# Kernel tuning notes

Hardware: AMD Instinct MI355X
Metric: run time of the kernel (lower is better)

Reference implementation:

```python
import jax, jax.numpy as jnp
import numpy as np
from jax import lax

B, T, C = 1, 2048, 2048
HS = 64
H = C // HS          # 32 heads
FFN = 7168
NS = 4               # packed sequences in the batch-1 stream
EPS_LN = 1e-5
EPS_GN = 1e-5 * 8 ** 2   # GroupNorm eps = 1e-5 * head_size_divisor**2


def setup_inputs() -> dict:
    key = jax.random.key(0)
    ks = iter(jax.random.split(key, 48))
    def rn(shape, s=1.0):
        return jax.random.normal(next(ks), shape, jnp.float32) * s
    sc = C ** -0.5
    return dict(
        x=rn((B, T, C)),
        start_pos=jnp.array([0, 512, 1024, 1536], dtype=jnp.int32),
        att_state=rn((NS, C)),
        wkv_state=rn((NS, H, HS, HS), 0.1),
        ffn_state=rn((NS, C)),
        ln1_g=jnp.ones((C,), jnp.float32), ln1_b=jnp.zeros((C,), jnp.float32),
        ln2_g=jnp.ones((C,), jnp.float32), ln2_b=jnp.zeros((C,), jnp.float32),
        tm_maa_x=rn((C,), 0.1), tm_maa_w=rn((C,), 0.1), tm_maa_k=rn((C,), 0.1),
        tm_maa_v=rn((C,), 0.1), tm_maa_r=rn((C,), 0.1), tm_maa_g=rn((C,), 0.1),
        tm_w1=rn((C, 160), 0.02), tm_w2=rn((5, 32, C), 0.02),
        td=rn((C,), 0.3) - 0.5, td_w1=rn((C, 64), 0.02), td_w2=rn((64, C), 0.02),
        u=rn((H, HS), 0.1),
        Wr=rn((C, C), sc), Wk=rn((C, C), sc), Wv=rn((C, C), sc),
        Wg=rn((C, C), sc), Wo=rn((C, C), sc),
        lnx_g=jnp.ones((C,), jnp.float32), lnx_b=jnp.zeros((C,), jnp.float32),
        cm_maa_k=rn((C,), 0.1), cm_maa_r=rn((C,), 0.1),
        Wck=rn((C, FFN), sc), Wcv=rn((FFN, C), FFN ** -0.5), Wcr=rn((C, C), sc),
    )


def _ln(x, g, b, eps):
    m = x.mean(-1, keepdims=True)
    v = ((x - m) ** 2).mean(-1, keepdims=True)
    return (x - m) * lax.rsqrt(v + eps) * g + b


def _shift(x, start_pos, state):
    # ZeroPad2d((0,0,1,-1)) token shift, then restore per-sequence carry state
    sh = jnp.concatenate([jnp.zeros_like(x[:, :1]), x[:, :-1]], axis=1)
    return sh.at[0, start_pos, :].set(state)


def reference(x, start_pos, att_state, wkv_state, ffn_state,
              ln1_g, ln1_b, ln2_g, ln2_b,
              tm_maa_x, tm_maa_w, tm_maa_k, tm_maa_v, tm_maa_r, tm_maa_g,
              tm_w1, tm_w2, td, td_w1, td_w2, u,
              Wr, Wk, Wv, Wg, Wo, lnx_g, lnx_b,
              cm_maa_k, cm_maa_r, Wck, Wcv, Wcr):
    is_start = jnp.zeros((T,), bool).at[start_pos].set(True)
    seq_id = jnp.clip(jnp.cumsum(is_start.astype(jnp.int32)) - 1, 0, NS - 1)

    # ---------------- Tmix (RWKV6 time mix) ----------------
    xa = _ln(x, ln1_g, ln1_b, EPS_LN)
    sh = _shift(xa, start_pos, att_state)
    xx = sh - xa
    xxx = jnp.tanh((xa + xx * tm_maa_x) @ tm_w1)                    # [B,T,160]
    mix = jnp.einsum('btse,sec->sbtc', xxx.reshape(B, T, 5, 32), tm_w2)
    mw, mk, mv, mr, mg = mix
    xw = xa + xx * (tm_maa_w + mw)
    xk = xa + xx * (tm_maa_k + mk)
    xv = xa + xx * (tm_maa_v + mv)
    xr = xa + xx * (tm_maa_r + mr)
    xg = xa + xx * (tm_maa_g + mg)
    r = (xr @ Wr).reshape(T, H, HS)
    k = (xk @ Wk).reshape(T, H, HS)
    v = (xv @ Wv).reshape(T, H, HS)
    g = jax.nn.silu(xg @ Wg)                                        # [B,T,C]
    w = td + jnp.tanh(xw @ td_w1) @ td_w2                           # [B,T,C]
    dec = jnp.exp(-jnp.exp(w)).reshape(T, H, HS)

    # continuous WKV recurrence: per-sequence state restore at starts
    def step(S, inp):
        rt, kt, vt, dt, st, sid = inp
        S = jnp.where(st, wkv_state[sid], S)                        # [H,HS,HS]
        y = jnp.einsum('hi,hij->hj', rt, S) \
            + (rt * u * kt).sum(-1, keepdims=True) * vt             # bonus term
        S = dt[:, :, None] * S + kt[:, :, None] * vt[:, None, :]
        return S, y

    _, y = lax.scan(step, jnp.zeros((H, HS, HS), jnp.float32),
                    (r, k, v, dec, is_start, seq_id))
    y = y.reshape(B, T, H, HS)
    # GroupNorm (n_head groups) fused per token/head
    mu = y.mean(-1, keepdims=True)
    var = ((y - mu) ** 2).mean(-1, keepdims=True)
    y = ((y - mu) * lax.rsqrt(var + EPS_GN)).reshape(B, T, C) * lnx_g + lnx_b
    x = x + (y * g) @ Wo

    # ---------------- CMix (channel mix) ----------------
    xf = _ln(x, ln2_g, ln2_b, EPS_LN)
    sh = _shift(xf, start_pos, ffn_state)
    xx = sh - xf
    xk = xf + xx * cm_maa_k
    xr = xf + xx * cm_maa_r
    kv = jnp.square(jax.nn.relu(xk @ Wck)) @ Wcv
    x = x + jax.nn.sigmoid(xr @ Wcr) * kv
    return x
```

## Files before the change

### kernel.cpp

```cpp
#include <hip/hip_runtime.h>
#include <stdint.h>


#define TT 2048
#define CC 2048
#define NH 32
#define HSZ 64
#define FFND 7168
#define CHUNK 32
#define NCHUNK 64

typedef __attribute__((ext_vector_type(8))) short short8;
typedef __attribute__((ext_vector_type(4))) float f32x4;

__device__ __forceinline__ float bf2f(short s){
  return __uint_as_float(((uint32_t)(uint16_t)s) << 16);
}
__device__ __forceinline__ short f2bf(float f){
  uint32_t u = __float_as_uint(f);
  u = u + 0x7fffu + ((u >> 16) & 1u);
  return (short)(u >> 16);
}

__global__ __launch_bounds__(256) void ln_kernel(
    const float* __restrict__ xin, const float* __restrict__ gam,
    const float* __restrict__ bet, float* __restrict__ out, float eps)
{
  int t = blockIdx.x, tid = threadIdx.x;
  const float* row = xin + (size_t)t*CC;
  float4 v0 = *(const float4*)(row + tid*8);
  float4 v1 = *(const float4*)(row + tid*8 + 4);
  float s  = v0.x+v0.y+v0.z+v0.w + v1.x+v1.y+v1.z+v1.w;
  float ss = v0.x*v0.x+v0.y*v0.y+v0.z*v0.z+v0.w*v0.w
           + v1.x*v1.x+v1.y*v1.y+v1.z*v1.z+v1.w*v1.w;
  #pragma unroll
  for(int off=1; off<64; off<<=1){ s += __shfl_xor(s,off); ss += __shfl_xor(ss,off); }
  __shared__ float sm[8];
  int w = tid>>6;
  if((tid&63)==0){ sm[w]=s; sm[4+w]=ss; }
  __syncthreads();
  s = sm[0]+sm[1]+sm[2]+sm[3]; ss = sm[4]+sm[5]+sm[6]+sm[7];
  float mean = s * (1.f/CC);
  float var  = ss * (1.f/CC) - mean*mean;
  float rstd = rsqrtf(var + eps);
  float* orow = out + (size_t)t*CC;
  int c = tid*8;
  float vv[8] = {v0.x,v0.y,v0.z,v0.w,v1.x,v1.y,v1.z,v1.w};
  #pragma unroll
  for(int j=0;j<8;j++) orow[c+j] = (vv[j]-mean)*rstd*gam[c+j] + bet[c+j];
}

__global__ __launch_bounds__(256) void ln2_fused_kernel(
    const float* __restrict__ p0, const float* __restrict__ p1,
    const float* __restrict__ xres, const float* __restrict__ gam,
    const float* __restrict__ bet, float* __restrict__ xsum,
    float* __restrict__ lnout, float eps)
{
  int t = blockIdx.x, tid = threadIdx.x;
  size_t base = (size_t)t*CC + tid*8;
  float vv[8];
  float s = 0.f, ss = 0.f;
  #pragma unroll
  for(int j=0;j<8;j++){
    float v = p0[base+j] + p1[base+j] + xres[base+j];
    vv[j] = v; s += v; ss += v*v;
    xsum[base+j] = v;
  }
  #pragma unroll
  for(int off=1; off<64; off<<=1){ s += __shfl_xor(s,off); ss += __shfl_xor(ss,off); }
  __shared__ float sm[8];
  int w = tid>>6;
  if((tid&63)==0){ sm[w]=s; sm[4+w]=ss; }
  __syncthreads();
  s = sm[0]+sm[1]+sm[2]+sm[3]; ss = sm[4]+sm[5]+sm[6]+sm[7];
  float mean = s * (1.f/CC);
  float var  = ss * (1.f/CC) - mean*mean;
  float rstd = rsqrtf(var + eps);
  int c = tid*8;
  #pragma unroll
  for(int j=0;j<8;j++) lnout[base+j] = (vv[j]-mean)*rstd*gam[c+j] + bet[c+j];
}

__global__ __launch_bounds__(256) void shift1_kernel(
    const float* __restrict__ xa, const float* __restrict__ st,
    const int* __restrict__ sp, float* __restrict__ xxb)
{
  int t = blockIdx.x, tid = threadIdx.x;
  int sp0=sp[0], sp1=sp[1], sp2=sp[2], sp3=sp[3];
  bool is_start = (sp0==t)|(sp1==t)|(sp2==t)|(sp3==t);
  int sid = (sp0<=t)+(sp1<=t)+(sp2<=t)+(sp3<=t) - 1;
  sid = sid<0?0:(sid>3?3:sid);
  int c = tid*8;
  const float* src = is_start ? (st + (size_t)sid*CC + c)
                   : (t>0 ? xa + (size_t)(t-1)*CC + c : nullptr);
  const float* cur = xa + (size_t)t*CC + c;
  float* o = xxb + (size_t)t*CC + c;
  #pragma unroll
  for(int jj=0;jj<8;jj++){
    float sh = src ? src[jj] : 0.f;
    o[jj] = sh - cur[jj];
  }
}

__global__ __launch_bounds__(256) void shift2_kernel(
    const float* __restrict__ xf, const float* __restrict__ st,
    const int* __restrict__ sp, const float* __restrict__ cmk,
    const float* __restrict__ cmr, short* __restrict__ xk2, short* __restrict__ xr2)
{
  int t = blockIdx.x, tid = threadIdx.x;
  int sp0=sp[0], sp1=sp[1], sp2=sp[2], sp3=sp[3];
  bool is_start = (sp0==t)|(sp1==t)|(sp2==t)|(sp3==t);
  int sid = (sp0<=t)+(sp1<=t)+(sp2<=t)+(sp3<=t) - 1;
  sid = sid<0?0:(sid>3?3:sid);
  int c = tid*8;
  const float* src = is_start ? (st + (size_t)sid*CC + c)
                   : (t>0 ? xf + (size_t)(t-1)*CC + c : nullptr);
  const float* cur = xf + (size_t)t*CC + c;
  size_t ix = (size_t)t*CC + c;
  #pragma unroll
  for(int jj=0;jj<8;jj++){
    float xfv = cur[jj];
    float sh = src ? src[jj] : 0.f;
    float d = sh - xfv;
    xk2[ix+jj] = f2bf(xfv + d*cmk[c+jj]);
    xr2[ix+jj] = f2bf(xfv + d*cmr[c+jj]);
  }
}

__global__ __launch_bounds__(256) void zprep_kernel(const float* __restrict__ xa,
   const float* __restrict__ xx, const float* __restrict__ maa, short* __restrict__ z)
{
  size_t i = ((size_t)blockIdx.x*256 + threadIdx.x)*8;
  int c = (int)(i & (CC-1));
  #pragma unroll
  for(int j=0;j<8;j++) z[i+j] = f2bf(xa[i+j] + xx[i+j]*maa[c+j]);
}

__global__ __launch_bounds__(256) void mix5_kernel(
    const float* __restrict__ xxxb, const float* __restrict__ w2,
    const float* __restrict__ xa, const float* __restrict__ xxv,
    const float* __restrict__ mw, const float* __restrict__ mk,
    const float* __restrict__ mv, const float* __restrict__ mr,
    const float* __restrict__ mg,
    short* __restrict__ ow, short* __restrict__ ok, short* __restrict__ ov,
    short* __restrict__ orr, short* __restrict__ og)
{
  int g = blockIdx.x*256 + threadIdx.x;
  int c = g & (CC-1);
  int t0 = (g >> 11) * 8;
  float acc[5][8];
  #pragma unroll
  for(int s=0;s<5;s++)
    #pragma unroll
    for(int tt=0;tt<8;tt++) acc[s][tt]=0.f;
  #pragma unroll
  for(int s=0;s<5;s++){
    for(int e=0;e<32;e++){
      float wv = w2[(size_t)(s*32+e)*CC + c];
      #pragma unroll
      for(int tt=0;tt<8;tt++)
        acc[s][tt] += xxxb[(size_t)(t0+tt)*160 + s*32 + e] * wv;
    }
  }
  float vmw=mw[c], vmk=mk[c], vmv=mv[c], vmr=mr[c], vmg=mg[c];
  #pragma unroll
  for(int tt=0;tt<8;tt++){
    size_t ix = (size_t)(t0+tt)*CC + c;
    float av = xa[ix], xv = xxv[ix];
    ow[ix]  = f2bf(av + xv*(vmw + acc[0][tt]));
    ok[ix]  = f2bf(av + xv*(vmk + acc[1][tt]));
    ov[ix]  = f2bf(av + xv*(vmv + acc[2][tt]));
    orr[ix] = f2bf(av + xv*(vmr + acc[3][tt]));
    og[ix]  = f2bf(av + xv*(vmg + acc[4][tt]));
  }
}

__global__ __launch_bounds__(256) void dec_kernel(
    const float* __restrict__ h1b, const float* __restrict__ tw2,
    const float* __restrict__ td, float* __restrict__ out)
{
  int g = blockIdx.x*256 + threadIdx.x;
  int c = g & (CC-1);
  int t0 = (g >> 11)*8;
  float acc[8] = {0,0,0,0,0,0,0,0};
  for(int e=0;e<64;e++){
    float wv = tw2[(size_t)e*CC + c];
    #pragma unroll
    for(int tt=0;tt<8;tt++) acc[tt] += h1b[(size_t)(t0+tt)*64 + e]*wv;
  }
  float tdc = td[c];
  #pragma unroll
  for(int tt=0;tt<8;tt++)
    out[(size_t)(t0+tt)*CC + c] = expf(-expf(tdc + acc[tt]));
}

template<int N, int NK>
__global__ __launch_bounds__(256) void tanh_reduce_kernel(
    const float* __restrict__ part, float* __restrict__ out)
{
  int idx = blockIdx.x*256 + threadIdx.x;
  int col = idx & (N-1);
  int row = idx >> (N==256 ? 8 : 7);
  float s = 0.f;
  #pragma unroll
  for(int z=0;z<8;z++) s += part[(size_t)z*TT*N + idx];
  if(col < NK) out[(size_t)row*NK + col] = tanhf(s);
}

__global__ __launch_bounds__(256) void transpose_f2bf_kernel(
    const float* __restrict__ W, short* __restrict__ Wt, int K, int N)
{
  __shared__ float tile[64][65];
  int n0 = blockIdx.x*64, k0 = blockIdx.y*64;
  int tid = threadIdx.x;
  #pragma unroll
  for(int q=0;q<16;q++){
    int ix = q*256 + tid;
    int r = ix >> 6, cc2 = ix & 63;
    tile[r][cc2] = (n0 + cc2 < N) ? W[(size_t)(k0+r)*N + n0 + cc2] : 0.f;
  }
  __syncthreads();
  #pragma unroll
  for(int q=0;q<16;q++){
    int ix = q*256 + tid;
    int r = ix >> 6, cc2 = ix & 63;
    Wt[(size_t)(n0+r)*K + k0 + cc2] = f2bf(tile[cc2][r]);
  }
}

struct WPtr4 { const float* w[4]; };
__global__ __launch_bounds__(256) void transpose4_f2bf_kernel(
    WPtr4 ws4, short* __restrict__ Wt)
{
  __shared__ float tile[64][65];
  int z = blockIdx.z;
  const float* W = ws4.w[z];
  short* dst = Wt + (size_t)z*CC*CC;
  int n0 = blockIdx.x*64, k0 = blockIdx.y*64;
  int tid = threadIdx.x;
  #pragma unroll
  for(int q=0;q<16;q++){
    int ix = q*256 + tid;
    int r = ix >> 6, cc2 = ix & 63;
    tile[r][cc2] = W[(size_t)(k0+r)*CC + n0 + cc2];
  }
  __syncthreads();
  #pragma unroll
  for(int q=0;q<16;q++){
    int ix = q*256 + tid;
    int r = ix >> 6, cc2 = ix & 63;
    dst[(size_t)(n0+r)*CC + k0 + cc2] = f2bf(tile[cc2][r]);
  }
}

__device__ __forceinline__ void load_lds16(const void* g, void* l){
  __builtin_amdgcn_global_load_lds(
      (const __attribute__((address_space(1))) uint32_t*)g,
      (__attribute__((address_space(3))) uint32_t*)l, 16, 0, 0);
}

template<int EPI>
__global__ __launch_bounds__(256) void gemm_bt_kernel(
    const short* __restrict__ A, const short* __restrict__ Bt,
    void* __restrict__ Cout, int M, int N, int Kstride, int Klen,
    long zA, long zB, long zC)
{
  __shared__ __align__(16) short As[128*64];
  __shared__ __align__(16) short Bs[128*64];
  int z = blockIdx.z;
  const short* A0 = A + (size_t)z*zA;
  const short* B0 = Bt + (size_t)z*zB;
  int tid = threadIdx.x;
  int w = tid >> 6, lane = tid & 63;
  int l16 = lane & 15, lhi = lane >> 4;
  int wr = w >> 1, wc = w & 1;
  int gx = gridDim.x;
  int nwg = gx*gridDim.y;
  int lin = blockIdx.y*gx + blockIdx.x;
  int wg = (lin & 7)*(nwg >> 3) + (lin >> 3);
  int bn = wg % gx, bm = wg / gx;
  const short* Ab = A0 + (size_t)bm*128*Kstride;
  const short* Bb = B0 + (size_t)bn*128*Kstride;
  int srow = w*8 + (lane>>3);
  int scol = lane & 7;
  f32x4 acc[4][4] = {};
  for(int kt=0; kt<Klen; kt+=64){
    __syncthreads();
    #pragma unroll
    for(int q=0;q<4;q++){
      int row = q*32 + srow;
      int c8 = scol ^ (row & 7);
      int ldsoff = (q*256 + w*64)*8;
      load_lds16(Ab + (size_t)row*Kstride + kt + c8*8, As + ldsoff);
      load_lds16(Bb + (size_t)row*Kstride + kt + c8*8, Bs + ldsoff);
    }
    __syncthreads();
    #pragma unroll
    for(int kk=0;kk<2;kk++){
      short8 af[4], bf[4];
      #pragma unroll
      for(int m=0;m<4;m++){
        int row = wr*64 + m*16 + l16;
        int slot = (kk*4 + lhi) ^ (row & 7);
        af[m] = *(const short8*)(As + row*64 + slot*8);
      }
      #pragma unroll
      for(int n=0;n<4;n++){
        int row = wc*64 + n*16 + l16;
        int slot = (kk*4 + lhi) ^ (row & 7);
        bf[n] = *(const short8*)(Bs + row*64 + slot*8);
      }
      #pragma unroll
      for(int m=0;m<4;m++){
        #pragma unroll
        for(int n=0;n<4;n++)
          acc[m][n] = __builtin_amdgcn_mfma_f32_16x16x32_bf16(af[m], bf[n], acc[m][n], 0, 0, 0);
      }
    }
  }
  int m0 = bm*128 + wr*64;
  int n0 = bn*128 + wc*64;
  #pragma unroll
  for(int m=0;m<4;m++){
    #pragma unroll
    for(int n=0;n<4;n++){
      #pragma unroll
      for(int jj=0;jj<4;jj++){
        int row = m0 + m*16 + lhi*4 + jj;
        int col = n0 + n*16 + l16;
        size_t ix = (size_t)row*N + col;
        float val = acc[m][n][jj];
        if constexpr (EPI==0){ ((short*)Cout)[(size_t)z*zC + ix] = f2bf(val); }
        else if constexpr (EPI==3){ float rv = fmaxf(val, 0.f); ((short*)Cout)[ix] = f2bf(rv*rv); }
        else if constexpr (EPI==5){ ((float*)Cout)[(size_t)z*zC + ix] = val; }
        else {
          short* o = (short*)Cout + (size_t)z*zC;
          o[ix] = (z==3) ? f2bf(val/(1.f+expf(-val))) : f2bf(val);
        }
      }
    }
  }
}

template<int EPI>
__global__ __launch_bounds__(512, 1) void gemm256_kernel(
    const short* __restrict__ A, const short* __restrict__ Bt,
    void* __restrict__ Cout, int M, int N, int Kstride, int Klen,
    long zA, long zB, long zC)
{
  __shared__ __align__(16) short As[2][256*64];
  __shared__ __align__(16) short Bs[2][256*64];
  int z = blockIdx.z;
  const short* A0 = A + (size_t)z*zA;
  const short* B0 = Bt + (size_t)z*zB;
  int tid = threadIdx.x;
  int w = tid >> 6, lane = tid & 63;
  int l16 = lane & 15, lhi = lane >> 4;
  int wr = w >> 2, wc = w & 3;
  int gx = gridDim.x;
  int nwg = gx*gridDim.y;
  int lin = blockIdx.y*gx + blockIdx.x;
  int wg = (lin & 7)*(nwg >> 3) + (lin >> 3);
  int bn = wg % gx, bm = wg / gx;
  const short* Ab = A0 + (size_t)bm*256*Kstride;
  const short* Bb = B0 + (size_t)bn*256*Kstride;
  int srow_w = w*8 + (lane>>3);
  int scol = lane & 7;
  f32x4 acc[8][4] = {};

  auto STAGE = [&](int kt, int b){
    #pragma unroll
    for(int q=0;q<4;q++){
      int row = q*64 + srow_w;
      int c8 = scol ^ (row & 7);
      int ldsoff = (q*64 + w*8)*64;
      load_lds16(Ab + (size_t)row*Kstride + kt + c8*8, &As[b][ldsoff]);
      load_lds16(Bb + (size_t)row*Kstride + kt + c8*8, &Bs[b][ldsoff]);
    }
  };

  int NT = Klen >> 6;
  int cur = 0;
  STAGE(0, 0);
  for(int t=0; t<NT; ++t){
    __builtin_amdgcn_sched_barrier(0);
    if(t+1 < NT){
      STAGE((t+1)<<6, cur^1);
      asm volatile("s_waitcnt vmcnt(8)" ::: "memory");
    } else {
      asm volatile("s_waitcnt vmcnt(0)" ::: "memory");
    }
    __builtin_amdgcn_s_barrier();
    __builtin_amdgcn_sched_barrier(0);
    const short* Ac = &As[cur][0];
    const short* Bc = &Bs[cur][0];
    short8 bfr[4][2];
    #pragma unroll
    for(int n=0;n<4;n++){
      #pragma unroll
      for(int kk=0;kk<2;kk++){
        int row = wc*64 + n*16 + l16;
        int slot = (kk*4 + lhi) ^ (row & 7);
        bfr[n][kk] = *(const short8*)(Bc + row*64 + slot*8);
      }
    }
    #pragma unroll
    for(int p=0;p<4;p++){
      short8 afr[2][2];
      #pragma unroll
      for(int mm=0;mm<2;mm++){
        #pragma unroll
        for(int kk=0;kk<2;kk++){
          int row = wr*128 + (p*2+mm)*16 + l16;
          int slot = (kk*4 + lhi) ^ (row & 7);
          afr[mm][kk] = *(const short8*)(Ac + row*64 + slot*8);
        }
      }
      __builtin_amdgcn_s_setprio(1);
      #pragma unroll
      for(int mm=0;mm<2;mm++){
        #pragma unroll
        for(int n=0;n<4;n++){
          #pragma unroll
          for(int kk=0;kk<2;kk++)
            acc[p*2+mm][n] = __builtin_amdgcn_mfma_f32_16x16x32_bf16(
                afr[mm][kk], bfr[n][kk], acc[p*2+mm][n], 0, 0, 0);
        }
      }
      __builtin_amdgcn_s_setprio(0);
      __builtin_amdgcn_s_barrier();
    }
    cur ^= 1;
  }
  int m0 = bm*256 + wr*128;
  int n0 = bn*256 + wc*64;
  #pragma unroll
  for(int m=0;m<8;m++){
    #pragma unroll
    for(int n=0;n<4;n++){
      #pragma unroll
      for(int jj=0;jj<4;jj++){
        int row = m0 + m*16 + lhi*4 + jj;
        int col = n0 + n*16 + l16;
        size_t ix = (size_t)row*N + col;
        float val = acc[m][n][jj];
        if constexpr (EPI==3){ float rv = fmaxf(val, 0.f); ((short*)Cout)[ix] = f2bf(rv*rv); }
        else if constexpr (EPI==5){ ((float*)Cout)[(size_t)z*zC + ix] = val; }
        else {
          short* o = (short*)Cout + (size_t)z*zC;
          o[ix] = (z==3) ? f2bf(val/(1.f+expf(-val))) : f2bf(val);
        }
      }
    }
  }
}

__global__ __launch_bounds__(256) void wkv_chunk_kernel(
    const short* __restrict__ rb, const short* __restrict__ kb,
    const short* __restrict__ vb, const float* __restrict__ db,
    const float* __restrict__ wkv_state, const float* __restrict__ u,
    const int* __restrict__ sp,
    float* __restrict__ yb, short* __restrict__ rtb,
    float* __restrict__ Bc, float* __restrict__ Pc)
{
  int blk = blockIdx.x;
  int ch = blk >> 5;
  int h  = blk & 31;
  int tid = threadIdx.x;
  int a = tid & 3, j = tid >> 2;
  int w = tid >> 6, lane = tid & 63;
  __shared__ float sr[2][64], sk[2][64], suk[2][64], sv[2][64], sd[2][64];
  __shared__ float sp_[64];
  float u_reg = (w==1) ? u[h*64 + lane] : 0.f;
  if(tid < 64) sp_[tid] = 1.f;
  float S[16];
  #pragma unroll
  for(int ii=0;ii<16;ii++) S[ii]=0.f;
  int sp0=sp[0], sp1=sp[1], sp2=sp[2], sp3=sp[3];
  int tbase = ch*CHUNK;
  {
    size_t gb = (size_t)tbase*CC + h*64;
    if(w==0)      sr[0][lane] = bf2f(rb[gb+lane]);
    else if(w==1){ float kv_=bf2f(kb[gb+lane]); sk[0][lane]=kv_; suk[0][lane]=u_reg*kv_; }
    else if(w==2) sv[0][lane] = bf2f(vb[gb+lane]);
    else          sd[0][lane] = db[gb+lane];
  }
  __syncthreads();
  for(int tl=0; tl<CHUNK; ++tl){
    int t = tbase + tl;
    int buf = tl & 1;
    if(tl+1 < CHUNK){
      size_t nb = (size_t)(t+1)*CC + h*64;
      int b2_ = buf^1;
      if(w==0)      sr[b2_][lane] = bf2f(rb[nb+lane]);
      else if(w==1){ float kv_=bf2f(kb[nb+lane]); sk[b2_][lane]=kv_; suk[b2_][lane]=u_reg*kv_; }
      else if(w==2) sv[b2_][lane] = bf2f(vb[nb+lane]);
      else          sd[b2_][lane] = db[nb+lane];
    }
    size_t base = (size_t)t*CC + h*64;
    bool is_start = (sp0==t)|(sp1==t)|(sp2==t)|(sp3==t);
    if(is_start){
      int sid = (sp0<=t)+(sp1<=t)+(sp2<=t)+(sp3<=t) - 1;
      sid = sid<0?0:(sid>3?3:sid);
      const float* wsrc = wkv_state + (((size_t)sid*NH + h)*HSZ + a*16)*HSZ + j;
      #pragma unroll
      for(int ii=0;ii<16;ii++) S[ii] = wsrc[(size_t)ii*HSZ];
      if(tid < 64) sp_[tid] = 0.f;
    }
    float vj = sv[buf][j];
    float yp = 0.f, bp = 0.f;
    #pragma unroll
    for(int ii=0;ii<16;ii++){
      int i = a*16 + ii;
      float ri = sr[buf][i];
      yp += ri * S[ii];
      bp += ri * suk[buf][i];
    }
    yp += __shfl_xor(yp, 1); yp += __shfl_xor(yp, 2);
    bp += __shfl_xor(bp, 1); bp += __shfl_xor(bp, 2);
    if(a == 0) yb[base + j] = yp + bp*vj;
    if(tid < 64){
      rtb[base + tid] = f2bf(sr[buf][tid] * sp_[tid]);
      sp_[tid] *= sd[buf][tid];
    }
    #pragma unroll
    for(int ii=0;ii<16;ii++){
      int i = a*16 + ii;
      S[ii] = sd[buf][i]*S[ii] + sk[buf][i]*vj;
    }
    __syncthreads();
  }
  size_t cb = ((size_t)ch*NH + h)*HSZ*HSZ;
  #pragma unroll
  for(int ii=0;ii<16;ii++) Bc[cb + (size_t)(a*16+ii)*HSZ + j] = S[ii];
  if(tid < 64) Pc[((size_t)ch*NH + h)*HSZ + tid] = sp_[tid];
}

__global__ __launch_bounds__(256) void wkv_combine_kernel(
    float* __restrict__ BS, const float* __restrict__ Pc)
{
  int idx = blockIdx.x*256 + threadIdx.x;
  int hi = idx >> 6;
  float s = 0.f;
  for(int cc=0; cc<NCHUNK; ++cc){
    size_t ix = (size_t)cc*(NH*HSZ*HSZ) + idx;
    float b = BS[ix];
    BS[ix] = s;
    s = Pc[cc*(NH*HSZ) + hi]*s + b;
  }
}

__global__ __launch_bounds__(256) void wkv_corr_kernel(
    const short* __restrict__ rtb, const float* __restrict__ Sin, float* __restrict__ yb)
{
  int blk = blockIdx.x;
  int ch = blk >> 5, h = blk & 31;
  __shared__ float Ssm[64][64];
  __shared__ float Rsm[32][65];
  int tid = threadIdx.x;
  const float* Sp = Sin + (size_t)(ch*NH + h)*HSZ*HSZ;
  #pragma unroll
  for(int q=0;q<16;q++) ((float*)Ssm)[q*256+tid] = Sp[q*256+tid];
  #pragma unroll
  for(int q=0;q<8;q++){
    int ix = q*256 + tid;
    int tl = ix>>6, i = ix&63;
    Rsm[tl][i] = bf2f(rtb[(size_t)(ch*CHUNK+tl)*CC + h*64 + i]);
  }
  __syncthreads();
  int tl = tid >> 3;
  int jq = tid & 7;
  float acc[8];
  #pragma unroll
  for(int jj=0;jj<8;jj++) acc[jj]=0.f;
  for(int i=0;i<64;i++){
    float rv = Rsm[tl][i];
    #pragma unroll
    for(int jj=0;jj<8;jj++) acc[jj] += rv * Ssm[i][jq*8+jj];
  }
  #pragma unroll
  for(int jj=0;jj<8;jj++)
    yb[(size_t)(ch*CHUNK+tl)*CC + h*64 + jq*8+jj] += acc[jj];
}

__global__ __launch_bounds__(256) void gn_mul_kernel(
    const float* __restrict__ yb, const short* __restrict__ gb,
    const float* __restrict__ gam, const float* __restrict__ bet,
    short* __restrict__ yg)
{
  int t = blockIdx.x, tid = threadIdx.x;
  int w = tid >> 6, lane = tid & 63;
  for(int q=0;q<8;q++){
    int h = q*4 + w;
    int cc = h*64 + lane;
    float val = yb[(size_t)t*CC + cc];
    float s = val, ss = val*val;
    #pragma unroll
    for(int off=1;off<64;off<<=1){ s += __shfl_xor(s,off); ss += __shfl_xor(ss,off); }
    float mu = s*(1.f/64.f);
    float var = ss*(1.f/64.f) - mu*mu;
    float rstd = rsqrtf(var + 6.4e-4f);
    float o = (val-mu)*rstd*gam[cc] + bet[cc];
    yg[(size_t)t*CC + cc] = f2bf(o * bf2f(gb[(size_t)t*CC + cc]));
  }
}

__global__ __launch_bounds__(256) void final_kernel(
    const float* __restrict__ s0, const float* __restrict__ s1,
    const float* __restrict__ kv0, const float* __restrict__ kv1,
    const float* __restrict__ kv2, const float* __restrict__ kv3,
    float* __restrict__ out)
{
  size_t i = ((size_t)blockIdx.x*256 + threadIdx.x)*8;
  #pragma unroll
  for(int j=0;j<8;j++){
    float sv = s0[i+j] + s1[i+j];
    float sig = 1.f/(1.f + expf(-sv));
    out[i+j] = out[i+j] + sig*(kv0[i+j] + kv1[i+j] + kv2[i+j] + kv3[i+j]);
  }
}

extern "C" void kernel_launch(void* const* d_in, const int* in_sizes, int n_in,
                              void* d_out, int out_size, void* d_ws, size_t ws_size,
                              hipStream_t stream)
{
  (void)in_sizes; (void)n_in; (void)out_size;
  const float* x         = (const float*)d_in[0];
  const int*   sp        = (const int*)d_in[1];
  const float* att_state = (const float*)d_in[2];
  const float* wkv_state = (const float*)d_in[3];
  const float* ffn_state = (const float*)d_in[4];
  const float* ln1_g=(const float*)d_in[5],  *ln1_b=(const float*)d_in[6];
  const float* ln2_g=(const float*)d_in[7],  *ln2_b=(const float*)d_in[8];
  const float* maa_x=(const float*)d_in[9],  *maa_w=(const float*)d_in[10], *maa_k=(const float*)d_in[11];
  const float* maa_v=(const float*)d_in[12], *maa_r=(const float*)d_in[13], *maa_g=(const float*)d_in[14];
  const float* tm_w1=(const float*)d_in[15], *tm_w2=(const float*)d_in[16];
  const float* td=(const float*)d_in[17],    *td_w1=(const float*)d_in[18], *td_w2=(const float*)d_in[19];
  const float* u = (const float*)d_in[20];
  const float* Wr=(const float*)d_in[21], *Wk=(const float*)d_in[22], *Wv=(const float*)d_in[23];
  const float* Wg=(const float*)d_in[24], *Wo=(const float*)d_in[25];
  const float* lnx_g=(const float*)d_in[26], *lnx_b=(const float*)d_in[27];
  const float* cm_k=(const float*)d_in[28],  *cm_r=(const float*)d_in[29];
  const float* Wck=(const float*)d_in[30], *Wcv=(const float*)d_in[31], *Wcr=(const float*)d_in[32];

  char* ws = (char*)d_ws;
  const size_t SLOT  = (size_t)TT*CC*4;
  const size_t BSLOT = (size_t)TT*CC*2;
  const size_t WT_SZ = (size_t)4*CC*CC*2;
  const size_t NEED  = 6*SLOT + 10*BSLOT + WT_SZ + (4u<<20);
  if(ws_size < NEED) return;

  float* xa   = (float*)(ws + 0*SLOT);
  float* xxb  = (float*)(ws + 1*SLOT);
  float* zw   = (float*)(ws + 2*SLOT);
  float* decb = (float*)(ws + 3*SLOT);
  float* yb   = (float*)(ws + 4*SLOT);
  float* S5   = (float*)(ws + 5*SLOT);
  float* BS   = xa;
  float* xxxPart = zw;
  float* h1Part  = yb;
  short* bA   = (short*)(ws + 6*SLOT);
  short* bO   = (short*)(ws + 6*SLOT + 4*BSLOT);
  short* b1 = bO + 0*(TT*CC);
  short* b2 = bO + 1*(TT*CC);
  short* b3 = bO + 2*(TT*CC);
  short* b4 = bO + 3*(TT*CC);
  short* b5 = bO + 4*(TT*CC);
  short* b6 = bO + 5*(TT*CC);
  short* WT = (short*)(ws + 6*SLOT + 10*BSLOT);
  char*  aux = (char*)WT + WT_SZ;
  float* xxxb = (float*)(aux);
  float* h1b  = (float*)(aux + (2u<<20));
  float* Pc   = (float*)(aux + (5u<<19));
  float* xmid = (float*)d_out;

  dim3 B256(256), B512(512);
  const int NTC8 = TT*CC/8/256;

  ln_kernel<<<TT, B256, 0, stream>>>(x, ln1_g, ln1_b, xa, 1e-5f);
  shift1_kernel<<<TT, B256, 0, stream>>>(xa, att_state, sp, xxb);
  zprep_kernel<<<NTC8, B256, 0, stream>>>(xa, xxb, maa_x, bA);
  transpose_f2bf_kernel<<<dim3(4, CC/64), B256, 0, stream>>>(tm_w1, WT, CC, 160);
  gemm_bt_kernel<5><<<dim3(2, TT/128, 8), B256, 0, stream>>>(bA, WT, xxxPart, TT, 256, CC, 256,
      256, 256, (long)TT*256);
  tanh_reduce_kernel<256,160><<<TT, B256, 0, stream>>>(xxxPart, xxxb);
  mix5_kernel<<<NTC8, B256, 0, stream>>>(xxxb, tm_w2, xa, xxb,
      maa_w, maa_k, maa_v, maa_r, maa_g,
      b5, bA + 1*(TT*CC), bA + 2*(TT*CC), bA, bA + 3*(TT*CC));
  transpose_f2bf_kernel<<<dim3(2, CC/64), B256, 0, stream>>>(td_w1, WT, CC, 64);
  gemm_bt_kernel<5><<<dim3(1, TT/128, 8), B256, 0, stream>>>(b5, WT, h1Part, TT, 128, CC, 256,
      256, 256, (long)TT*128);
  tanh_reduce_kernel<128,64><<<TT/2, B256, 0, stream>>>(h1Part, h1b);
  dec_kernel<<<NTC8, B256, 0, stream>>>(h1b, td_w2, td, decb);

  WPtr4 w4; w4.w[0]=Wr; w4.w[1]=Wk; w4.w[2]=Wv; w4.w[3]=Wg;
  transpose4_f2bf_kernel<<<dim3(CC/64, CC/64, 4), B256, 0, stream>>>(w4, WT);
  gemm256_kernel<6><<<dim3(CC/256, TT/256, 4), B512, 0, stream>>>(bA, WT, b1, TT, CC, CC, CC,
      (long)TT*CC, (long)CC*CC, (long)TT*CC);

  wkv_chunk_kernel<<<NCHUNK*NH, B256, 0, stream>>>(b1, b2, b3, decb, wkv_state, u, sp,
                                                   yb, b5, BS, Pc);
  wkv_combine_kernel<<<NH*HSZ*HSZ/256, B256, 0, stream>>>(BS, Pc);
  wkv_corr_kernel<<<NCHUNK*NH, B256, 0, stream>>>(b5, BS, yb);
  gn_mul_kernel<<<TT, B256, 0, stream>>>(yb, b4, lnx_g, lnx_b, b6);

  transpose_f2bf_kernel<<<dim3(CC/64, CC/64), B256, 0, stream>>>(Wo, WT, CC, CC);
  gemm_bt_kernel<5><<<dim3(CC/128, TT/128, 2), B256, 0, stream>>>(b6, WT, yb, TT, CC, CC, 1024,
      1024, 1024, (long)TT*CC);
  ln2_fused_kernel<<<TT, B256, 0, stream>>>(yb, S5, x, ln2_g, ln2_b, xmid, zw, 1e-5f);

  shift2_kernel<<<TT, B256, 0, stream>>>(zw, ffn_state, sp, cm_k, cm_r, bA, bA + 1*(TT*CC));
  transpose_f2bf_kernel<<<dim3(FFND/64, CC/64), B256, 0, stream>>>(Wck, WT, CC, FFND);
  gemm256_kernel<3><<<dim3(FFND/256, TT/256, 1), B512, 0, stream>>>(bA, WT, b1, TT, FFND, CC, CC,
      0, 0, 0);
  transpose_f2bf_kernel<<<dim3(CC/64, FFND/64), B256, 0, stream>>>(Wcv, WT, FFND, CC);
  gemm256_kernel<5><<<dim3(CC/256, TT/256, 4), B512, 0, stream>>>(b1, WT, zw, TT, CC, FFND, 1792,
      1792, 1792, (long)TT*CC);
  transpose_f2bf_kernel<<<dim3(CC/64, CC/64), B256, 0, stream>>>(Wcr, WT, CC, CC);
  gemm_bt_kernel<5><<<dim3(CC/128, TT/128, 2), B256, 0, stream>>>(bA + 1*(TT*CC), WT, xa, TT, CC, CC, 1024,
      1024, 1024, (long)TT*CC);
  final_kernel<<<NTC8, B256, 0, stream>>>(xa, xxb, zw, decb, yb, S5, xmid);
}
```

Baseline: 792.4 us.

## Restructure GEMM main loop into finer-grained interleaved load/compute phases

The 256x256 bf16 GEMM main loop is rewritten to process two K-tiles per iteration. Global-to-LDS staging of A and B is split into half-tile pieces, and each piece is issued between the four MFMA phases. This spreads memory traffic across the compute and is meant to hide load latency better than the previous single prefetch of the whole next tile. It adds more barriers per K-tile and relies on hand-placed vmcnt waits and an even number of K-tiles, so a miscount could cause stalls or races.

```diff
diff --git a/kernel.cpp b/kernel.cpp
--- a/kernel.cpp
+++ b/kernel.cpp
@@ -368,70 +368,100 @@
   int scol = lane & 7;
   f32x4 acc[8][4] = {};
 
-  auto STAGE = [&](int kt, int b){
-    #pragma unroll
-    for(int q=0;q<4;q++){
-      int row = q*64 + srow_w;
+  auto STG = [&](const short* src, short* dst, int half, int kt){
+    #pragma unroll
+    for(int q=0;q<2;q++){
+      int row = half*128 + q*64 + srow_w;
       int c8 = scol ^ (row & 7);
-      int ldsoff = (q*64 + w*8)*64;
-      load_lds16(Ab + (size_t)row*Kstride + kt + c8*8, &As[b][ldsoff]);
-      load_lds16(Bb + (size_t)row*Kstride + kt + c8*8, &Bs[b][ldsoff]);
+      load_lds16(src + (size_t)row*Kstride + kt + c8*8,
+                 dst + (half*128 + q*64 + w*8)*64);
     }
   };
-
-  int NT = Klen >> 6;
-  int cur = 0;
-  STAGE(0, 0);
-  for(int t=0; t<NT; ++t){
-    __builtin_amdgcn_sched_barrier(0);
-    if(t+1 < NT){
-      STAGE((t+1)<<6, cur^1);
-      asm volatile("s_waitcnt vmcnt(8)" ::: "memory");
-    } else {
-      asm volatile("s_waitcnt vmcnt(0)" ::: "memory");
-    }
-    __builtin_amdgcn_s_barrier();
-    __builtin_amdgcn_sched_barrier(0);
-    const short* Ac = &As[cur][0];
-    const short* Bc = &Bs[cur][0];
-    short8 bfr[4][2];
-    #pragma unroll
-    for(int n=0;n<4;n++){
+  auto DSA = [&](const short* Ac, int p, short8 afr[2][2]){
+    #pragma unroll
+    for(int mm=0;mm<2;mm++)
+      #pragma unroll
+      for(int kk=0;kk<2;kk++){
+        int row = wr*128 + (p*2+mm)*16 + l16;
+        int slot = (kk*4 + lhi) ^ (row & 7);
+        afr[mm][kk] = *(const short8*)(Ac + row*64 + slot*8);
+      }
+  };
+  auto DSB = [&](const short* Bc, short8 bfr[4][2]){
+    #pragma unroll
+    for(int n=0;n<4;n++)
       #pragma unroll
       for(int kk=0;kk<2;kk++){
         int row = wc*64 + n*16 + l16;
         int slot = (kk*4 + lhi) ^ (row & 7);
         bfr[n][kk] = *(const short8*)(Bc + row*64 + slot*8);
       }
-    }
-    #pragma unroll
-    for(int p=0;p<4;p++){
-      short8 afr[2][2];
-      #pragma unroll
-      for(int mm=0;mm<2;mm++){
+  };
+  auto MM = [&](int p, short8 afr[2][2], short8 bfr[4][2]){
+    __builtin_amdgcn_s_setprio(1);
+    #pragma unroll
+    for(int mm=0;mm<2;mm++)
+      #pragma unroll
+      for(int n=0;n<4;n++)
         #pragma unroll
-        for(int kk=0;kk<2;kk++){
-          int row = wr*128 + (p*2+mm)*16 + l16;
-          int slot = (kk*4 + lhi) ^ (row & 7);
-          afr[mm][kk] = *(const short8*)(Ac + row*64 + slot*8);
-        }
-      }
-      __builtin_amdgcn_s_setprio(1);
-      #pragma unroll
-      for(int mm=0;mm<2;mm++){
-        #pragma unroll
-        for(int n=0;n<4;n++){
-          #pragma unroll
-          for(int kk=0;kk<2;kk++)
-            acc[p*2+mm][n] = __builtin_amdgcn_mfma_f32_16x16x32_bf16(
-                afr[mm][kk], bfr[n][kk], acc[p*2+mm][n], 0, 0, 0);
-        }
-      }
-      __builtin_amdgcn_s_setprio(0);
-      __builtin_amdgcn_s_barrier();
-    }
-    cur ^= 1;
-  }
+        for(int kk=0;kk<2;kk++)
+          acc[p*2+mm][n] = __builtin_amdgcn_mfma_f32_16x16x32_bf16(
+              afr[mm][kk], bfr[n][kk], acc[p*2+mm][n], 0, 0, 0);
+    __builtin_amdgcn_s_setprio(0);
+  };
+  #define PH_SYNC() do{ __builtin_amdgcn_s_barrier(); \
+      asm volatile("s_waitcnt lgkmcnt(0)" ::: "memory"); \
+      __builtin_amdgcn_sched_barrier(0); }while(0)
+  #define PH_END() do{ __builtin_amdgcn_s_barrier(); \
+      __builtin_amdgcn_sched_barrier(0); }while(0)
+
+  int NT = Klen >> 6;
+  int niter = NT >> 1;
+  STG(Ab, &As[0][0], 0, 0); STG(Ab, &As[0][0], 1, 0);
+  STG(Bb, &Bs[0][0], 0, 0); STG(Bb, &Bs[0][0], 1, 0);
+  STG(Bb, &Bs[1][0], 0, 64); STG(Bb, &Bs[1][0], 1, 64);
+  asm volatile("s_waitcnt vmcnt(4)" ::: "memory");
+  __builtin_amdgcn_s_barrier();
+  __builtin_amdgcn_sched_barrier(0);
+
+  for(int i=0;i<niter;++i){
+    int kt_o  = (2*i+1) << 6;
+    int kt_e2 = (2*i+2) << 6;
+    int kt_o2 = (2*i+3) << 6;
+    bool st = (i+1 < niter);
+    short8 bfr[4][2], afr[2][2];
+    DSB(&Bs[0][0], bfr);
+    DSA(&As[0][0], 0, afr);
+    STG(Ab, &As[1][0], 0, kt_o);
+    PH_SYNC(); MM(0, afr, bfr); PH_END();
+    DSA(&As[0][0], 1, afr);
+    STG(Ab, &As[1][0], 1, kt_o);
+    PH_SYNC(); MM(1, afr, bfr); PH_END();
+    DSA(&As[0][0], 2, afr);
+    if(st) STG(Bb, &Bs[0][0], 0, kt_e2);
+    PH_SYNC(); MM(2, afr, bfr); PH_END();
+    DSA(&As[0][0], 3, afr);
+    if(st) STG(Bb, &Bs[0][0], 1, kt_e2);
+    asm volatile("s_waitcnt vmcnt(4)" ::: "memory");
+    PH_SYNC(); MM(3, afr, bfr); PH_END();
+    DSB(&Bs[1][0], bfr);
+    DSA(&As[1][0], 0, afr);
+    if(st) STG(Ab, &As[0][0], 0, kt_e2);
+    PH_SYNC(); MM(0, afr, bfr); PH_END();
+    DSA(&As[1][0], 1, afr);
+    if(st) STG(Ab, &As[0][0], 1, kt_e2);
+    PH_SYNC(); MM(1, afr, bfr); PH_END();
+    DSA(&As[1][0], 2, afr);
+    if(st) STG(Bb, &Bs[1][0], 0, kt_o2);
+    PH_SYNC(); MM(2, afr, bfr); PH_END();
+    DSA(&As[1][0], 3, afr);
+    if(st) STG(Bb, &Bs[1][0], 1, kt_o2);
+    asm volatile("s_waitcnt vmcnt(4)" ::: "memory");
+    PH_SYNC(); MM(3, afr, bfr); PH_END();
+  }
+  #undef PH_SYNC
+  #undef PH_END
+
   int m0 = bm*256 + wr*128;
   int n0 = bn*256 + wc*64;
   #pragma unroll
```

Result: faster. 764.5 us (-3.5%).
